# Kernel tuning notes

Hardware: AMD Instinct MI355X
Metric: run time of the kernel (lower is better)

The kernel has to match this reference:

```python
import jax, jax.numpy as jnp
import numpy as np

N_NODES = 100000
N_EDGES = 1600000
D = 128          # in_dim == out_dim
H = 8            # num_heads
DH = D // H      # head dim = 16
DFF = 2 * D
EPS_LN = 1e-5


def _ln(x, g, b):
    mu = jnp.mean(x, axis=-1, keepdims=True)
    var = jnp.var(x, axis=-1, keepdims=True)
    return (x - mu) * jax.lax.rsqrt(var + EPS_LN) * g + b


def setup_inputs() -> dict:
    key = jax.random.key(0)
    ks = jax.random.split(key, 12)
    s = 1.0 / np.sqrt(D)
    inp = {
        "h": jax.random.normal(ks[0], (N_NODES, D), jnp.float32),
        "src": jax.random.randint(ks[1], (N_EDGES,), 0, N_NODES, jnp.int32),
        "dst": jax.random.randint(ks[2], (N_EDGES,), 0, N_NODES, jnp.int32),
        "Wq": jax.random.normal(ks[3], (D, D), jnp.float32) * s,
        "Wk": jax.random.normal(ks[4], (D, D), jnp.float32) * s,
        "Wv": jax.random.normal(ks[5], (D, D), jnp.float32) * s,
        "Wo": jax.random.normal(ks[6], (D, D), jnp.float32) * s,
        "bo": jnp.zeros((D,), jnp.float32),
        "ln1_g": jnp.ones((D,), jnp.float32),
        "ln1_b": jnp.zeros((D,), jnp.float32),
        "W1": jax.random.normal(ks[7], (D, DFF), jnp.float32) * s,
        "b1": jnp.zeros((DFF,), jnp.float32),
        "W2": jax.random.normal(ks[8], (DFF, D), jnp.float32) * (1.0 / np.sqrt(DFF)),
        "b2": jnp.zeros((D,), jnp.float32),
        "ln2_g": jnp.ones((D,), jnp.float32),
        "ln2_b": jnp.zeros((D,), jnp.float32),
    }
    return inp


def reference(h, src, dst, Wq, Wk, Wv, Wo, bo, ln1_g, ln1_b, W1, b1, W2, b2, ln2_g, ln2_b):
    n = h.shape[0]
    # Q/K/V projections (no bias), split into heads: [N, H, DH]
    Q = (h @ Wq).reshape(n, H, DH)
    K = (h @ Wk).reshape(n, H, DH)
    V = (h @ Wv).reshape(n, H, DH)

    # edge-wise attention score: K[src] . Q[dst] / sqrt(DH), exp-clamped
    score = jnp.einsum("ehd,ehd->eh", K[src], Q[dst]) / np.sqrt(DH)  # [E, H]
    score = jnp.exp(jnp.clip(score, -5.0, 5.0))

    # weighted message sum + normalizer via segment reduce over dst
    m = V[src] * score[:, :, None]                                   # [E, H, DH]
    wV = jax.ops.segment_sum(m, dst, num_segments=n)                 # [N, H, DH]
    z = jax.ops.segment_sum(score, dst, num_segments=n)              # [N, H]

    h_attn = (wV / (z[:, :, None] + 1e-6)).reshape(n, D)

    # output projection + residual + LN
    x = h + (h_attn @ Wo + bo)
    x = _ln(x, ln1_g, ln1_b)

    # FFN + residual + LN
    y = jax.nn.relu(x @ W1 + b1) @ W2 + b2
    x = _ln(x + y, ln2_g, ln2_b)
    return x
```

## Files before the change

### kernel.cpp

```cpp
#include <hip/hip_runtime.h>
#include <hip/hip_bf16.h>
#include <math.h>


typedef __attribute__((ext_vector_type(8))) short bf16x8;
typedef __attribute__((ext_vector_type(4))) float f32x4;
typedef __attribute__((ext_vector_type(2))) _Float16 half2_t;

#define BSHIFT 9
#define BSIZE  512
#define KVROW  384

static __device__ __forceinline__ half2_t h2(unsigned u) {
    return __builtin_bit_cast(half2_t, u);
}
static __device__ __forceinline__ float bl(unsigned u) {
    return __uint_as_float(u << 16);
}
static __device__ __forceinline__ float bh(unsigned u) {
    return __uint_as_float(u & 0xffff0000u);
}

__global__ __launch_bounds__(256)
void qkv_fused(const float* __restrict__ h,
               const __hip_bfloat16* __restrict__ Wqt,
               const __hip_bfloat16* __restrict__ Wkt,
               const __hip_bfloat16* __restrict__ Wvt,
               unsigned short* __restrict__ Qh,
               unsigned char* __restrict__ KV,
               int N)
{
    __shared__ unsigned short As[64 * 136];
    __shared__ unsigned short Bs[128 * 136];

    const int tid  = threadIdx.x;
    const int row0 = blockIdx.x * 64;
    const int wave = tid >> 6, lane = tid & 63;
    const int quad = lane >> 4, l15 = lane & 15;

    #pragma unroll
    for (int it = 0; it < 4; ++it) {
        int i = tid + it * 256;
        int r = i >> 4, kb = i & 15;
        int rg = row0 + r; if (rg > N - 1) rg = N - 1;
        const float4 f0 = *(const float4*)&h[(size_t)rg * 128 + kb * 8];
        const float4 f1 = *(const float4*)&h[(size_t)rg * 128 + kb * 8 + 4];
        __hip_bfloat162 b01 = __float22bfloat162_rn(make_float2(f0.x, f0.y));
        __hip_bfloat162 b23 = __float22bfloat162_rn(make_float2(f0.z, f0.w));
        __hip_bfloat162 b45 = __float22bfloat162_rn(make_float2(f1.x, f1.y));
        __hip_bfloat162 b67 = __float22bfloat162_rn(make_float2(f1.z, f1.w));
        uint4 u;
        u.x = *(unsigned*)&b01; u.y = *(unsigned*)&b23;
        u.z = *(unsigned*)&b45; u.w = *(unsigned*)&b67;
        *(uint4*)&As[r * 136 + kb * 8] = u;
    }

    const __hip_bfloat16* Ws[3] = { Wqt, Wkt, Wvt };

    #pragma unroll
    for (int w = 0; w < 3; ++w) {
        #pragma unroll
        for (int it = 0; it < 8; ++it) {
            int i = tid + it * 256;
            int r = i >> 4, kb = i & 15;
            *(uint4*)&Bs[r * 136 + kb * 8] =
                *(const uint4*)&Ws[w][(size_t)r * 128 + kb * 8];
        }
        __syncthreads();

        f32x4 acc[8];
        #pragma unroll
        for (int t = 0; t < 8; ++t) acc[t] = (f32x4)0.f;

        const unsigned short* ap = &As[(wave * 16 + l15) * 136 + quad * 8];
        const unsigned short* bp = &Bs[l15 * 136 + quad * 8];
        #pragma unroll
        for (int ks = 0; ks < 4; ++ks) {
            bf16x8 a = *(const bf16x8*)(ap + ks * 32);
            #pragma unroll
            for (int t = 0; t < 8; ++t) {
                bf16x8 b = *(const bf16x8*)(bp + t * 16 * 136 + ks * 32);
                acc[t] = __builtin_amdgcn_mfma_f32_16x16x32_bf16(a, b, acc[t], 0, 0, 0);
            }
        }
        __syncthreads();

        const int rbase = row0 + wave * 16 + quad * 4;
        #pragma unroll
        for (int i = 0; i < 4; ++i) {
            int row = rbase + i;
            if (row >= N) continue;
            #pragma unroll
            for (int t = 0; t < 8; ++t) {
                float v = acc[t][i];
                if (w == 0) {
                    ((_Float16*)Qh)[(size_t)row * 128 + t * 16 + l15] = (_Float16)v;
                } else if (w == 1) {
                    int pk = __builtin_amdgcn_cvt_pk_fp8_f32(v, 0.f, 0, false);
                    KV[(size_t)row * KVROW + t * 16 + l15] = (unsigned char)(pk & 0xff);
                } else {
                    *(__hip_bfloat16*)(KV + (size_t)row * KVROW + 128 +
                                       (t * 16 + l15) * 2) = __float2bfloat16(v);
                }
            }
        }
    }
}

template<int K, int YLOOP, bool RELU, bool LN, bool RESID, bool BIAS>
__global__ __launch_bounds__(256)
void gemm_mfma(const __hip_bfloat16* __restrict__ Ab, int lda,
               const __hip_bfloat16* __restrict__ Bt, int ldbt,
               const float* __restrict__ bias, const float* __restrict__ resid,
               const float* __restrict__ lng, const float* __restrict__ lnb,
               float* __restrict__ Cf, __hip_bfloat16* __restrict__ Cb, int ldc,
               int N)
{
    constexpr int CK = 128;
    static_assert(YLOOP == 1 || K == CK, "YLOOP>1 needs single K chunk");
    __shared__ unsigned short As[64 * 136];
    __shared__ unsigned short Bs[128 * 136];

    const int tid  = threadIdx.x;
    const int row0 = blockIdx.x * 64;
    const int wave = tid >> 6, lane = tid & 63;
    const int quad = lane >> 4, l15 = lane & 15;
    const int rbase = row0 + wave * 16 + quad * 4;

    for (int yy = 0; yy < YLOOP; ++yy) {
        const int col0 = yy * 128;

        f32x4 acc[8];
        #pragma unroll
        for (int t = 0; t < 8; ++t) acc[t] = (f32x4)0.f;

        for (int kc = 0; kc < K; kc += CK) {
            if (yy == 0) {
                #pragma unroll
                for (int it = 0; it < 4; ++it) {
                    int i = tid + it * 256;
                    int r = i >> 4, kb = i & 15;
                    int rg = row0 + r; if (rg > N - 1) rg = N - 1;
                    *(uint4*)&As[r * 136 + kb * 8] =
                        *(const uint4*)&Ab[(size_t)rg * lda + kc + kb * 8];
                }
            }
            #pragma unroll
            for (int it = 0; it < 8; ++it) {
                int i = tid + it * 256;
                int r = i >> 4, kb = i & 15;
                *(uint4*)&Bs[r * 136 + kb * 8] =
                    *(const uint4*)&Bt[(size_t)(col0 + r) * ldbt + kc + kb * 8];
            }
            __syncthreads();
            const unsigned short* ap = &As[(wave * 16 + l15) * 136 + quad * 8];
            const unsigned short* bp = &Bs[l15 * 136 + quad * 8];
            #pragma unroll
            for (int ks = 0; ks < 4; ++ks) {
                bf16x8 a = *(const bf16x8*)(ap + ks * 32);
                #pragma unroll
                for (int t = 0; t < 8; ++t) {
                    bf16x8 b = *(const bf16x8*)(bp + t * 16 * 136 + ks * 32);
                    acc[t] = __builtin_amdgcn_mfma_f32_16x16x32_bf16(a, b, acc[t], 0, 0, 0);
                }
            }
            __syncthreads();
        }

        float vals[8][4];
        #pragma unroll
        for (int t = 0; t < 8; ++t) {
            float bv = BIAS ? bias[col0 + t * 16 + l15] : 0.f;
            #pragma unroll
            for (int i = 0; i < 4; ++i) vals[t][i] = acc[t][i] + bv;
        }
        if (RESID) {
            #pragma unroll
            for (int i = 0; i < 4; ++i) {
                int row = rbase + i;
                if (row < N) {
                    #pragma unroll
                    for (int t = 0; t < 8; ++t)
                        vals[t][i] += resid[(size_t)row * 128 + t * 16 + l15];
                }
            }
        }
        if (RELU) {
            #pragma unroll
            for (int t = 0; t < 8; ++t)
                #pragma unroll
                for (int i = 0; i < 4; ++i) vals[t][i] = fmaxf(vals[t][i], 0.f);
        }
        if (LN) {
            #pragma unroll
            for (int i = 0; i < 4; ++i) {
                float s = 0.f, sq = 0.f;
                #pragma unroll
                for (int t = 0; t < 8; ++t) { float v = vals[t][i]; s += v; sq += v * v; }
                s  += __shfl_xor(s, 1);  s  += __shfl_xor(s, 2);
                s  += __shfl_xor(s, 4);  s  += __shfl_xor(s, 8);
                sq += __shfl_xor(sq, 1); sq += __shfl_xor(sq, 2);
                sq += __shfl_xor(sq, 4); sq += __shfl_xor(sq, 8);
                float m  = s * (1.f / 128.f);
                float rs = rsqrtf(sq * (1.f / 128.f) - m * m + 1e-5f);
                #pragma unroll
                for (int t = 0; t < 8; ++t) {
                    float g = lng[t * 16 + l15], b = lnb[t * 16 + l15];
                    vals[t][i] = (vals[t][i] - m) * rs * g + b;
                }
            }
        }
        #pragma unroll
        for (int i = 0; i < 4; ++i) {
            int row = rbase + i;
            if (row >= N) continue;
            if (Cf) {
                #pragma unroll
                for (int t = 0; t < 8; ++t)
                    Cf[(size_t)row * ldc + col0 + t * 16 + l15] = vals[t][i];
            }
            if (Cb) {
                #pragma unroll
                for (int t = 0; t < 8; ++t)
                    Cb[(size_t)row * ldc + col0 + t * 16 + l15] =
                        __float2bfloat16(vals[t][i]);
            }
        }
    }
}

struct WArgs {
    const float* src[6];
    __hip_bfloat16* dst[6];
    int R[6], C[6];
};
__global__ __launch_bounds__(256)
void cast_w(WArgs wa, int* __restrict__ bCnt)
{
    if (blockIdx.x == 0 && blockIdx.y == 0) bCnt[threadIdx.x] = 0;
    int w = blockIdx.y;
    int R = wa.R[w], C = wa.C[w];
    int i = blockIdx.x * 256 + threadIdx.x;
    if (i >= R * C) return;
    int sh = (C == 256) ? 8 : 7;
    int r = i >> sh, c = i & (C - 1);
    wa.dst[w][(size_t)c * R + r] = __float2bfloat16(wa.src[w][i]);
}

__global__ __launch_bounds__(256)
void bucket_hist(const int* __restrict__ dst, int* __restrict__ bCnt,
                 int E, int chunk, int NB)
{
    __shared__ int bh[256];
    const int t = threadIdx.x;
    bh[t] = 0;
    __syncthreads();
    const int s0 = blockIdx.x * chunk;
    const int s1 = min(E, s0 + chunk);
    for (int i = s0 + t; i < s1; i += 256)
        atomicAdd(&bh[dst[i] >> BSHIFT], 1);
    __syncthreads();
    if (t < NB && bh[t]) atomicAdd(&bCnt[t], bh[t]);
}

__global__ __launch_bounds__(256)
void bucket_scan(const int* __restrict__ bCnt, int* __restrict__ bBase,
                 int* __restrict__ gCur, int* __restrict__ rowStart,
                 int N, int E, int NB)
{
    __shared__ int wsum[4];
    const int t = threadIdx.x, lane = t & 63, wv = t >> 6;
    int v = (t < NB) ? bCnt[t] : 0;
    const int s = v;
    for (int off = 1; off < 64; off <<= 1) {
        int u = __shfl_up(v, off);
        if (lane >= off) v += u;
    }
    if (lane == 63) wsum[wv] = v;
    __syncthreads();
    int add = 0;
    for (int w = 0; w < wv; ++w) add += wsum[w];
    const int excl = v + add - s;
    if (t <= NB) bBase[t] = excl;
    if (t < NB)  gCur[t]  = excl;
    if (t == 0)  rowStart[N] = E;
}

__global__ __launch_bounds__(256)
void partition_kernel(const int* __restrict__ src, const int* __restrict__ dst,
                      int* __restrict__ gCur, uint2* __restrict__ P,
                      int E, int chunk, int NB)
{
    __shared__ int ch[256];
    __shared__ int cur[256];
    const int t = threadIdx.x;
    ch[t] = 0;
    __syncthreads();
    const int s0 = blockIdx.x * chunk;
    const int s1 = min(E, s0 + chunk);
    for (int i = s0 + t; i < s1; i += 256)
        atomicAdd(&ch[dst[i] >> BSHIFT], 1);
    __syncthreads();
    if (t < NB) {
        int c = ch[t];
        cur[t] = c ? atomicAdd(&gCur[t], c) : 0;
    }
    __syncthreads();
    for (int i = s0 + t; i < s1; i += 256) {
        int d = dst[i];
        int pos = atomicAdd(&cur[d >> BSHIFT], 1);
        P[pos] = make_uint2((unsigned)src[i], (unsigned)d);
    }
}

__global__ __launch_bounds__(256)
void bucket_scatter(const uint2* __restrict__ P, const int* __restrict__ bBase,
                    int* __restrict__ rowStart, int* __restrict__ esrc, int N)
{
    __shared__ int hist[BSIZE];
    __shared__ int cur[BSIZE];
    __shared__ int wsum[4];

    const int b  = blockIdx.x;
    const int t  = threadIdx.x;
    const int d0 = b << BSHIFT;
    const int bb  = bBase[b];
    const int cnt = bBase[b + 1] - bb;

    hist[t] = 0; hist[t + 256] = 0;
    __syncthreads();
    for (int i = t; i < cnt; i += 256)
        atomicAdd(&hist[(int)P[bb + i].y - d0], 1);
    __syncthreads();

    {
        const int a0 = hist[2 * t], a1 = hist[2 * t + 1];
        int v = a0 + a1;
        const int s = v;
        const int lane = t & 63, wv = t >> 6;
        for (int off = 1; off < 64; off <<= 1) {
            int u = __shfl_up(v, off);
            if (lane >= off) v += u;
        }
        if (lane == 63) wsum[wv] = v;
        __syncthreads();
        int add = 0;
        for (int w = 0; w < wv; ++w) add += wsum[w];
        const int exclT = v + add - s;
        cur[2 * t]     = exclT;
        cur[2 * t + 1] = exclT + a0;
    }
    __syncthreads();
    for (int i = t; i < BSIZE; i += 256) {
        int d = d0 + i;
        if (d < N) rowStart[d] = bb + cur[i];
    }
    __syncthreads();
    for (int i = t; i < cnt; i += 256) {
        uint2 p = P[bb + i];
        int pos = atomicAdd(&cur[(int)p.y - d0], 1);
        esrc[bb + pos] = (int)p.x;
    }
}

__global__ __launch_bounds__(256)
void aggregate_kernel(unsigned short* __restrict__ Qp,
                      const unsigned char* __restrict__ KV,
                      const int* __restrict__ esrc,
                      const int* __restrict__ rowStart, int N)
{
    const int lane = threadIdx.x & 63;
    const int wid  = threadIdx.x >> 6;
    const int d    = blockIdx.x * 4 + wid;
    if (d >= N) return;

    const int c = lane & 15;
    const int g = lane >> 4;

    const uint4 qraw = *(const uint4*)(Qp + (size_t)d * 128u + c * 8);
    const half2_t q0 = h2(qraw.x), q1 = h2(qraw.y),
                  q2 = h2(qraw.z), q3 = h2(qraw.w);
    const float qf0 = (float)q0.x, qf1 = (float)q0.y;
    const float qf2 = (float)q1.x, qf3 = (float)q1.y;
    const float qf4 = (float)q2.x, qf5 = (float)q2.y;
    const float qf6 = (float)q3.x, qf7 = (float)q3.y;

    const int beg = rowStart[d];
    const int end = rowStart[d + 1];
    const int endm1 = end - 1;

    float a0 = 0.f, a1 = 0.f, a2 = 0.f, a3 = 0.f;
    float a4 = 0.f, a5 = 0.f, a6 = 0.f, a7 = 0.f, z = 0.f;
    const float S = 0.36067376022224085f;
    const float C = 7.2134752044448170f;

    const int nIt = (end - beg + 7) >> 3;
    #pragma unroll 2
    for (int it = 0; it < nIt; ++it) {
        const int ea = beg + it * 8 + g;
        const int eb = ea + 4;
        const bool va = ea < end;
        const bool vb = eb < end;
        const int sa = esrc[va ? ea : endm1];
        const int sb = esrc[vb ? eb : endm1];
        const unsigned char* pa = KV + (size_t)(unsigned)sa * (size_t)KVROW;
        const unsigned char* pb = KV + (size_t)(unsigned)sb * (size_t)KVROW;
        const uint2 ka = *(const uint2*)(pa + c * 8);
        const uint4 vra = *(const uint4*)(pa + 128 + c * 16);
        const uint2 kb = *(const uint2*)(pb + c * 8);
        const uint4 vrb = *(const uint4*)(pb + 128 + c * 16);

        auto ka01 = __builtin_amdgcn_cvt_pk_f32_fp8(ka.x, false);
        auto ka23 = __builtin_amdgcn_cvt_pk_f32_fp8(ka.x, true);
        auto ka45 = __builtin_amdgcn_cvt_pk_f32_fp8(ka.y, false);
        auto ka67 = __builtin_amdgcn_cvt_pk_f32_fp8(ka.y, true);
        float p = ka01[0] * qf0 + ka01[1] * qf1 + ka23[0] * qf2 + ka23[1] * qf3
                + ka45[0] * qf4 + ka45[1] * qf5 + ka67[0] * qf6 + ka67[1] * qf7;
        p += __shfl_xor(p, 1);
        float se = exp2f(fminf(C, fmaxf(-C, p * S)));
        se = va ? se : 0.f;

        auto kb01 = __builtin_amdgcn_cvt_pk_f32_fp8(kb.x, false);
        auto kb23 = __builtin_amdgcn_cvt_pk_f32_fp8(kb.x, true);
        auto kb45 = __builtin_amdgcn_cvt_pk_f32_fp8(kb.y, false);
        auto kb67 = __builtin_amdgcn_cvt_pk_f32_fp8(kb.y, true);
        float p2 = kb01[0] * qf0 + kb01[1] * qf1 + kb23[0] * qf2 + kb23[1] * qf3
                 + kb45[0] * qf4 + kb45[1] * qf5 + kb67[0] * qf6 + kb67[1] * qf7;
        p2 += __shfl_xor(p2, 1);
        float se2 = exp2f(fminf(C, fmaxf(-C, p2 * S)));
        se2 = vb ? se2 : 0.f;

        a0 += bl(vra.x) * se; a1 += bh(vra.x) * se;
        a2 += bl(vra.y) * se; a3 += bh(vra.y) * se;
        a4 += bl(vra.z) * se; a5 += bh(vra.z) * se;
        a6 += bl(vra.w) * se; a7 += bh(vra.w) * se;
        z  += se;

        a0 += bl(vrb.x) * se2; a1 += bh(vrb.x) * se2;
        a2 += bl(vrb.y) * se2; a3 += bh(vrb.y) * se2;
        a4 += bl(vrb.z) * se2; a5 += bh(vrb.z) * se2;
        a6 += bl(vrb.w) * se2; a7 += bh(vrb.w) * se2;
        z  += se2;
    }

    a0 += __shfl_xor(a0, 16); a1 += __shfl_xor(a1, 16);
    a2 += __shfl_xor(a2, 16); a3 += __shfl_xor(a3, 16);
    a4 += __shfl_xor(a4, 16); a5 += __shfl_xor(a5, 16);
    a6 += __shfl_xor(a6, 16); a7 += __shfl_xor(a7, 16);
    z  += __shfl_xor(z, 16);
    a0 += __shfl_xor(a0, 32); a1 += __shfl_xor(a1, 32);
    a2 += __shfl_xor(a2, 32); a3 += __shfl_xor(a3, 32);
    a4 += __shfl_xor(a4, 32); a5 += __shfl_xor(a5, 32);
    a6 += __shfl_xor(a6, 32); a7 += __shfl_xor(a7, 32);
    z  += __shfl_xor(z, 32);

    if (g == 0) {
        const float inv = 1.0f / (z + 1e-6f);
        __hip_bfloat162 p0 = __float22bfloat162_rn(make_float2(a0 * inv, a1 * inv));
        __hip_bfloat162 p1 = __float22bfloat162_rn(make_float2(a2 * inv, a3 * inv));
        __hip_bfloat162 p2 = __float22bfloat162_rn(make_float2(a4 * inv, a5 * inv));
        __hip_bfloat162 p3 = __float22bfloat162_rn(make_float2(a6 * inv, a7 * inv));
        uint4 o;
        o.x = *(unsigned*)&p0; o.y = *(unsigned*)&p1;
        o.z = *(unsigned*)&p2; o.w = *(unsigned*)&p3;
        *(uint4*)(Qp + (size_t)d * 128u + c * 8) = o;
    }
}

extern "C" void kernel_launch(void* const* d_in, const int* in_sizes, int n_in,
                              void* d_out, int out_size, void* d_ws, size_t ws_size,
                              hipStream_t stream)
{
    const float* h    = (const float*)d_in[0];
    const int*   src  = (const int*)  d_in[1];
    const int*   dst  = (const int*)  d_in[2];
    const float* Wq   = (const float*)d_in[3];
    const float* Wk   = (const float*)d_in[4];
    const float* Wv   = (const float*)d_in[5];
    const float* Wo   = (const float*)d_in[6];
    const float* bo   = (const float*)d_in[7];
    const float* ln1g = (const float*)d_in[8];
    const float* ln1b = (const float*)d_in[9];
    const float* W1   = (const float*)d_in[10];
    const float* b1   = (const float*)d_in[11];
    const float* W2   = (const float*)d_in[12];
    const float* b2   = (const float*)d_in[13];
    const float* ln2g = (const float*)d_in[14];
    const float* ln2b = (const float*)d_in[15];

    const int N = in_sizes[0] / 128;
    const int E = in_sizes[1];
    const int NB = (N + BSIZE - 1) >> BSHIFT;

    unsigned short* Qh = (unsigned short*)d_ws;
    unsigned char*  KVc = (unsigned char*)(Qh + (size_t)N * 128);
    __hip_bfloat16* Xh = (__hip_bfloat16*)(KVc + (size_t)N * KVROW);
    float*          Xf = (float*)(Xh + (size_t)N * 128);
    __hip_bfloat16* Wt = (__hip_bfloat16*)(Xf + (size_t)N * 128);
    __hip_bfloat16* Wqt = Wt;
    __hip_bfloat16* Wkt = Wqt + 16384;
    __hip_bfloat16* Wvt = Wkt + 16384;
    __hip_bfloat16* Wot = Wvt + 16384;
    __hip_bfloat16* W1t = Wot + 16384;
    __hip_bfloat16* W2t = W1t + 32768;
    int* ib       = (int*)(W2t + 32768);
    int* bCnt     = ib;
    int* bBase    = ib + 256;
    int* gCur     = ib + 514;
    int* rowStart = ib + 770;
    int* esrc     = ib + 770 + N + 2;
    uint2* P      = (uint2*)Xf;
    __hip_bfloat16* Th = (__hip_bfloat16*)Qh;

    const dim3 blk(256);
    const int  nb    = (N + 63) / 64;
    const int  chunk = (E + 255) / 256;

    WArgs wa;
    wa.src[0] = Wq; wa.src[1] = Wk; wa.src[2] = Wv; wa.src[3] = Wo; wa.src[4] = W1; wa.src[5] = W2;
    wa.dst[0] = Wqt; wa.dst[1] = Wkt; wa.dst[2] = Wvt; wa.dst[3] = Wot; wa.dst[4] = W1t; wa.dst[5] = W2t;
    wa.R[0] = wa.R[1] = wa.R[2] = wa.R[3] = 128; wa.R[4] = 128; wa.R[5] = 256;
    wa.C[0] = wa.C[1] = wa.C[2] = wa.C[3] = 128; wa.C[4] = 256; wa.C[5] = 128;
    cast_w<<<dim3(128, 6), blk, 0, stream>>>(wa, bCnt);

    qkv_fused<<<dim3(nb), blk, 0, stream>>>(h, Wqt, Wkt, Wvt, Qh, KVc, N);

    bucket_hist<<<dim3(256), blk, 0, stream>>>(dst, bCnt, E, chunk, NB);
    bucket_scan<<<dim3(1), blk, 0, stream>>>(bCnt, bBase, gCur, rowStart, N, E, NB);
    partition_kernel<<<dim3(256), blk, 0, stream>>>(src, dst, gCur, P, E, chunk, NB);
    bucket_scatter<<<dim3(NB), blk, 0, stream>>>(P, bBase, rowStart, esrc, N);

    aggregate_kernel<<<dim3((N + 3) / 4), blk, 0, stream>>>(Qh, KVc, esrc, rowStart, N);

    gemm_mfma<128,1,false,true,true,true><<<dim3(nb), blk, 0, stream>>>(
        (const __hip_bfloat16*)Qh, 128, Wot, 128, bo, h, ln1g, ln1b, Xf, Xh, 128, N);

    gemm_mfma<128,2,true,false,false,true><<<dim3(nb), blk, 0, stream>>>(
        Xh, 128, W1t, 128, b1, nullptr, nullptr, nullptr, nullptr, Th, 256, N);

    gemm_mfma<256,1,false,true,true,true><<<dim3(nb), blk, 0, stream>>>(
        Th, 256, W2t, 256, b2, Xf, ln2g, ln2b, (float*)d_out, nullptr, 128, N);
}
```

Before: 391.2 us.

## Fuse FFN up/down projections and second LayerNorm into one kernel

```diff
diff --git a/kernel.cpp b/kernel.cpp
--- a/kernel.cpp
+++ b/kernel.cpp
@@ -226,6 +226,142 @@
                         __float2bfloat16(vals[t][i]);
             }
         }
+    }
+}
+
+__global__ __launch_bounds__(256)
+void ffn_fused(const __hip_bfloat16* __restrict__ Xh,
+               const __hip_bfloat16* __restrict__ W1t,
+               const __hip_bfloat16* __restrict__ W2t,
+               const float* __restrict__ b1, const float* __restrict__ b2,
+               const float* __restrict__ lng, const float* __restrict__ lnb,
+               float* __restrict__ out, int N)
+{
+    constexpr int SA = 130;
+    __shared__ unsigned short As[64 * SA];
+    __shared__ unsigned short Bs[128 * SA];
+    __shared__ unsigned short Ts[64 * SA];
+
+    const int tid  = threadIdx.x;
+    const int row0 = blockIdx.x * 64;
+    const int wave = tid >> 6, lane = tid & 63;
+    const int quad = lane >> 4, l15 = lane & 15;
+    const int rbase = row0 + wave * 16 + quad * 4;
+
+    #pragma unroll
+    for (int it = 0; it < 4; ++it) {
+        int i = tid + it * 256;
+        int r = i >> 4, kb = i & 15;
+        int rg = row0 + r; if (rg > N - 1) rg = N - 1;
+        *(uint4*)&As[r * SA + kb * 8] =
+            *(const uint4*)&Xh[(size_t)rg * 128 + kb * 8];
+    }
+
+    f32x4 acc2[8];
+    #pragma unroll
+    for (int t = 0; t < 8; ++t) acc2[t] = (f32x4)0.f;
+
+    #pragma unroll
+    for (int half = 0; half < 2; ++half) {
+        #pragma unroll
+        for (int it = 0; it < 8; ++it) {
+            int i = tid + it * 256;
+            int r = i >> 4, kb = i & 15;
+            *(uint4*)&Bs[r * SA + kb * 8] =
+                *(const uint4*)&W1t[(size_t)(half * 128 + r) * 128 + kb * 8];
+        }
+        __syncthreads();
+
+        f32x4 acc1[8];
+        #pragma unroll
+        for (int t = 0; t < 8; ++t) acc1[t] = (f32x4)0.f;
+        {
+            const unsigned short* ap = &As[(wave * 16 + l15) * SA + quad * 8];
+            const unsigned short* bp = &Bs[l15 * SA + quad * 8];
+            #pragma unroll
+            for (int ks = 0; ks < 4; ++ks) {
+                bf16x8 a = *(const bf16x8*)(ap + ks * 32);
+                #pragma unroll
+                for (int t = 0; t < 8; ++t) {
+                    bf16x8 b = *(const bf16x8*)(bp + t * 16 * SA + ks * 32);
+                    acc1[t] = __builtin_amdgcn_mfma_f32_16x16x32_bf16(a, b, acc1[t], 0, 0, 0);
+                }
+            }
+        }
+        __syncthreads();
+
+        #pragma unroll
+        for (int t = 0; t < 8; ++t) {
+            float bv = b1[half * 128 + t * 16 + l15];
+            #pragma unroll
+            for (int i = 0; i < 4; ++i) {
+                float v = fmaxf(acc1[t][i] + bv, 0.f);
+                __hip_bfloat16 hbv = __float2bfloat16(v);
+                Ts[(wave * 16 + quad * 4 + i) * SA + t * 16 + l15] =
+                    *(unsigned short*)&hbv;
+            }
+        }
+
+        #pragma unroll
+        for (int it = 0; it < 8; ++it) {
+            int i = tid + it * 256;
+            int r = i >> 4, kb = i & 15;
+            *(uint4*)&Bs[r * SA + kb * 8] =
+                *(const uint4*)&W2t[(size_t)r * 256 + half * 128 + kb * 8];
+        }
+        __syncthreads();
+
+        {
+            const unsigned short* ap = &Ts[(wave * 16 + l15) * SA + quad * 8];
+            const unsigned short* bp = &Bs[l15 * SA + quad * 8];
+            #pragma unroll
+            for (int ks = 0; ks < 4; ++ks) {
+                bf16x8 a = *(const bf16x8*)(ap + ks * 32);
+                #pragma unroll
+                for (int t = 0; t < 8; ++t) {
+                    bf16x8 b = *(const bf16x8*)(bp + t * 16 * SA + ks * 32);
+                    acc2[t] = __builtin_amdgcn_mfma_f32_16x16x32_bf16(a, b, acc2[t], 0, 0, 0);
+                }
+            }
+        }
+        __syncthreads();
+    }
+
+    float vals[8][4];
+    #pragma unroll
+    for (int t = 0; t < 8; ++t) {
+        float bv = b2[t * 16 + l15];
+        #pragma unroll
+        for (int i = 0; i < 4; ++i) {
+            float xr = __uint_as_float(
+                (unsigned)As[(wave * 16 + quad * 4 + i) * SA + t * 16 + l15] << 16);
+            vals[t][i] = acc2[t][i] + bv + xr;
+        }
+    }
+    #pragma unroll
+    for (int i = 0; i < 4; ++i) {
+        float s = 0.f, sq = 0.f;
+        #pragma unroll
+        for (int t = 0; t < 8; ++t) { float v = vals[t][i]; s += v; sq += v * v; }
+        s  += __shfl_xor(s, 1);  s  += __shfl_xor(s, 2);
+        s  += __shfl_xor(s, 4);  s  += __shfl_xor(s, 8);
+        sq += __shfl_xor(sq, 1); sq += __shfl_xor(sq, 2);
+        sq += __shfl_xor(sq, 4); sq += __shfl_xor(sq, 8);
+        float m  = s * (1.f / 128.f);
+        float rs = rsqrtf(sq * (1.f / 128.f) - m * m + 1e-5f);
+        #pragma unroll
+        for (int t = 0; t < 8; ++t) {
+            float g = lng[t * 16 + l15], b = lnb[t * 16 + l15];
+            vals[t][i] = (vals[t][i] - m) * rs * g + b;
+        }
+    }
+    #pragma unroll
+    for (int i = 0; i < 4; ++i) {
+        int row = rbase + i;
+        if (row >= N) continue;
+        #pragma unroll
+        for (int t = 0; t < 8; ++t)
+            out[(size_t)row * 128 + t * 16 + l15] = vals[t][i];
     }
 }
 
@@ -495,8 +631,7 @@
     unsigned short* Qh = (unsigned short*)d_ws;
     unsigned char*  KVc = (unsigned char*)(Qh + (size_t)N * 128);
     __hip_bfloat16* Xh = (__hip_bfloat16*)(KVc + (size_t)N * KVROW);
-    float*          Xf = (float*)(Xh + (size_t)N * 128);
-    __hip_bfloat16* Wt = (__hip_bfloat16*)(Xf + (size_t)N * 128);
+    __hip_bfloat16* Wt = (__hip_bfloat16*)(Xh + (size_t)N * 128);
     __hip_bfloat16* Wqt = Wt;
     __hip_bfloat16* Wkt = Wqt + 16384;
     __hip_bfloat16* Wvt = Wkt + 16384;
@@ -509,8 +644,7 @@
     int* gCur     = ib + 514;
     int* rowStart = ib + 770;
     int* esrc     = ib + 770 + N + 2;
-    uint2* P      = (uint2*)Xf;
-    __hip_bfloat16* Th = (__hip_bfloat16*)Qh;
+    uint2* P      = (uint2*)Xh;
 
     const dim3 blk(256);
     const int  nb    = (N + 63) / 64;
@@ -533,11 +667,9 @@
     aggregate_kernel<<<dim3((N + 3) / 4), blk, 0, stream>>>(Qh, KVc, esrc, rowStart, N);
 
     gemm_mfma<128,1,false,true,true,true><<<dim3(nb), blk, 0, stream>>>(
-        (const __hip_bfloat16*)Qh, 128, Wot, 128, bo, h, ln1g, ln1b, Xf, Xh, 128, N);
-
-    gemm_mfma<128,2,true,false,false,true><<<dim3(nb), blk, 0, stream>>>(
-        Xh, 128, W1t, 128, b1, nullptr, nullptr, nullptr, nullptr, Th, 256, N);
-
-    gemm_mfma<256,1,false,true,true,true><<<dim3(nb), blk, 0, stream>>>(
-        Th, 256, W2t, 256, b2, Xf, ln2g, ln2b, (float*)d_out, nullptr, 128, N);
-}
+        (const __hip_bfloat16*)Qh, 128, Wot, 128, bo, h, ln1g, ln1b,
+        nullptr, Xh, 128, N);
+
+    ffn_fused<<<dim3(nb), blk, 0, stream>>>(
+        Xh, W1t, W2t, b1, b2, ln2g, ln2b, (float*)d_out, N);
+}
```

Result: slower. 463.7 us (+18.5%).
